# Kernel optimization log

Measured on AMD Instinct MI355X. Metric: run time of the kernel, lower is better.

## Reference

```python
import jax, jax.numpy as jnp
import numpy as np

B, S, D = 2, 2048, 1024
H, L = 16, 64  # num_heads, latent_dim (head dim); head_dim = H*L = 1024
ROPE_BASE = 10000.0


def _rope_tables(seq_len, dim):
    inv_freq = 1.0 / (ROPE_BASE ** (2.0 * jnp.arange(0, dim // 2, dtype=jnp.float32) / dim))
    pos = jnp.arange(seq_len, dtype=jnp.float32)
    ang = pos[:, None] * inv_freq[None, :]           # [S, L/2]
    cos = jnp.cos(ang).reshape(1, seq_len, 1, dim // 2)
    sin = jnp.sin(ang).reshape(1, seq_len, 1, dim // 2)
    return cos, sin


def _apply_rope(t, cos, sin):
    # t: [B, S, H, L]; interleaved-pair rotation then concat halves (as in source)
    tr = t.reshape(*t.shape[:-1], -1, 2)             # [B,S,H,L/2,2]
    x0, x1 = tr[..., 0], tr[..., 1]
    out = jnp.concatenate([x0 * cos - x1 * sin, x0 * sin + x1 * cos], axis=-1)
    return out.reshape(t.shape)


def setup_inputs() -> dict:
    key = jax.random.key(0)
    ks = jax.random.split(key, 5)
    scale = 0.03  # ~xavier for 1024x1024
    return {
        "x": jax.random.normal(ks[0], (B, S, D), dtype=jnp.float32),
        "Wq": jax.random.normal(ks[1], (D, H * L), dtype=jnp.float32) * scale,
        "bq": jnp.zeros((H * L,), dtype=jnp.float32),
        "Wk": jax.random.normal(ks[2], (D, H * L), dtype=jnp.float32) * scale,
        "bk": jnp.zeros((H * L,), dtype=jnp.float32),
        "Wv": jax.random.normal(ks[3], (D, H * L), dtype=jnp.float32) * scale,
        "bv": jnp.zeros((H * L,), dtype=jnp.float32),
        "Wo": jax.random.normal(ks[4], (H * L, D), dtype=jnp.float32) * scale,
        "bo": jnp.zeros((D,), dtype=jnp.float32),
    }


def reference(x, Wq, bq, Wk, bk, Wv, bv, Wo, bo):
    b, s, _ = x.shape
    q = (x @ Wq + bq).reshape(b, s, H, L)
    k = (x @ Wk + bk).reshape(b, s, H, L)
    v = (x @ Wv + bv).reshape(b, s, H, L)
    cos, sin = _rope_tables(s, L)
    q = _apply_rope(q, cos, sin)
    k = _apply_rope(k, cos, sin)
    q = jnp.transpose(q, (0, 2, 1, 3))  # [B,H,S,L]
    k = jnp.transpose(k, (0, 2, 1, 3))
    v = jnp.transpose(v, (0, 2, 1, 3))
    scores = jnp.einsum('bnqd,bnkd->bnqk', q, k) / jnp.sqrt(jnp.float32(L))
    # causal mask: keep positions where key <= query
    causal = jnp.arange(s)[None, :] <= jnp.arange(s)[:, None]  # [S,S]
    scores = jnp.where(causal, scores, -1e9)
    attn = jax.nn.softmax(scores, axis=-1)
    attended = jnp.einsum('bnqk,bnkd->bnqd', attn, v)
    attended = jnp.transpose(attended, (0, 2, 1, 3)).reshape(b, s, H * L)
    return attended @ Wo + bo
```

## Files before the change

### kernel.cpp

```cpp
#include <hip/hip_runtime.h>
#include <hip/hip_bf16.h>

typedef __bf16 bf16_t;
typedef __bf16 bf16x2 __attribute__((ext_vector_type(2)));
typedef __bf16 bf16x4 __attribute__((ext_vector_type(4)));
typedef __bf16 bf16x8 __attribute__((ext_vector_type(8)));
typedef float  f32x4  __attribute__((ext_vector_type(4)));

#define GLDS16(gp, lp) __builtin_amdgcn_global_load_lds( \
    (const __attribute__((address_space(1))) void*)(gp), \
    (__attribute__((address_space(3))) void*)(lp), 16, 0, 0)

#define MFMA16(a, b, c) __builtin_amdgcn_mfma_f32_16x16x32_bf16((a), (b), (c), 0, 0, 0)

static constexpr int kB = 2, kS = 2048, kD = 1024, kH = 16, kL = 64;
static constexpr int kM = kB * kS;
static constexpr int kNqkv = 3 * kD;
static constexpr int kBH = kB * kH;

__global__ __launch_bounds__(256)
void prep_kernel(const float* __restrict__ x, bf16_t* __restrict__ xb,
                 const float* __restrict__ Wq, const float* __restrict__ Wk,
                 const float* __restrict__ Wv, const float* __restrict__ Wo,
                 bf16_t* __restrict__ Wqkv, bf16_t* __restrict__ WoT,
                 float* __restrict__ cosT, float* __restrict__ sinT) {
    const int bid = blockIdx.x;
    const int tid = threadIdx.x;
    if (bid < 4096) {
        int i = bid * 256 + tid;
        float4 v = ((const float4*)x)[i];
        bf16x4 o;
        o[0] = (bf16_t)v.x; o[1] = (bf16_t)v.y; o[2] = (bf16_t)v.z; o[3] = (bf16_t)v.w;
        ((bf16x4*)xb)[i] = o;
    } else if (bid < 8192) {
        __shared__ float t[32 * 33];
        const int wid4 = bid - 4096;
        const int z = wid4 >> 10;
        const int rem = wid4 & 1023;
        const int k0 = (rem & 31) * 32, n0 = (rem >> 5) * 32;
        const float* W = (z == 0) ? Wq : (z == 1) ? Wk : (z == 2) ? Wv : Wo;
        bf16_t* Wt = (z < 3) ? (Wqkv + (size_t)z * 1024 * 1024) : WoT;
#pragma unroll
        for (int i = 0; i < 4; ++i) {
            int idx = i * 256 + tid;
            int r = idx >> 5, c = idx & 31;
            t[r * 33 + c] = W[(size_t)(k0 + r) * 1024 + n0 + c];
        }
        __syncthreads();
#pragma unroll
        for (int i = 0; i < 4; ++i) {
            int idx = i * 256 + tid;
            int r = idx >> 5, c = idx & 31;
            Wt[(size_t)(n0 + r) * 1024 + k0 + c] = (bf16_t)t[c * 33 + r];
        }
    } else {
        int i = (bid - 8192) * 256 + tid;
        int s = i >> 5, j = i & 31;
        double inv = pow(10000.0, -2.0 * (double)j / 64.0);
        double ang = (double)s * inv;
        cosT[i] = (float)cos(ang);
        sinT[i] = (float)sin(ang);
    }
}

template <int MODE>
__global__ __launch_bounds__(256, 2)
void gemm_bf16(const bf16_t* __restrict__ A, const bf16_t* __restrict__ Bt,
               void* __restrict__ Cout,
               const float* __restrict__ b0, const float* __restrict__ b1,
               const float* __restrict__ b2, int Ndim, int Kdim) {
    __shared__ __align__(16) bf16_t Alds[128 * 32];
    __shared__ __align__(16) bf16_t Blds[128 * 32];
    const int tid = threadIdx.x;
    const int lane = tid & 63;
    const int wid = tid >> 6;
    const int lo = lane & 15, hi = lane >> 4;
    const int bm = blockIdx.x, bn = blockIdx.y;
    const int wr = wid >> 1, wc = wid & 1;

    const int rowS = (wid * 2) * 16 + (lane >> 2);
    const int colE = (lane & 3) * 8;
    const bf16_t* gA0 = A + (size_t)(bm * 128 + rowS) * Kdim + colE;
    const bf16_t* gA1 = gA0 + (size_t)16 * Kdim;
    const bf16_t* gB0 = Bt + (size_t)(bn * 128 + rowS) * Kdim + colE;
    const bf16_t* gB1 = gB0 + (size_t)16 * Kdim;
    bf16_t* lA0 = &Alds[(wid * 2) * 512];
    bf16_t* lA1 = &Alds[(wid * 2 + 1) * 512];
    bf16_t* lB0 = &Blds[(wid * 2) * 512];
    bf16_t* lB1 = &Blds[(wid * 2 + 1) * 512];

    f32x4 acc[4][4];
#pragma unroll
    for (int m = 0; m < 4; ++m)
#pragma unroll
        for (int n = 0; n < 4; ++n) acc[m][n] = (f32x4){0.f, 0.f, 0.f, 0.f};

    const int nk = Kdim >> 5;
    for (int kt = 0; kt < nk; ++kt) {
        const int k0 = kt * 32;
        GLDS16(gA0 + k0, lA0);
        GLDS16(gA1 + k0, lA1);
        GLDS16(gB0 + k0, lB0);
        GLDS16(gB1 + k0, lB1);
        __syncthreads();
        bf16x8 aF[4], bF[4];
#pragma unroll
        for (int m = 0; m < 4; ++m)
            aF[m] = *(const bf16x8*)&Alds[(wr * 64 + m * 16 + lo) * 32 + hi * 8];
#pragma unroll
        for (int n = 0; n < 4; ++n)
            bF[n] = *(const bf16x8*)&Blds[(wc * 64 + n * 16 + lo) * 32 + hi * 8];
#pragma unroll
        for (int m = 0; m < 4; ++m)
#pragma unroll
            for (int n = 0; n < 4; ++n)
                acc[m][n] = MFMA16(aF[m], bF[n], acc[m][n]);
        __syncthreads();
    }

    const int rbase = bm * 128 + wr * 64 + hi * 4;
    const int cbase = bn * 128 + wc * 64 + lo;
    if (MODE == 0) {
        bf16_t* C = (bf16_t*)Cout;
#pragma unroll
        for (int m = 0; m < 4; ++m)
#pragma unroll
            for (int n = 0; n < 4; ++n) {
                const int col = cbase + n * 16;
                const float bias = (col < 1024) ? b0[col]
                                 : (col < 2048) ? b1[col - 1024] : b2[col - 2048];
#pragma unroll
                for (int r = 0; r < 4; ++r) {
                    const int row = rbase + m * 16 + r;
                    C[(size_t)row * Ndim + col] = (bf16_t)(acc[m][n][r] + bias);
                }
            }
    } else {
        float* C = (float*)Cout;
#pragma unroll
        for (int m = 0; m < 4; ++m)
#pragma unroll
            for (int n = 0; n < 4; ++n) {
                const int col = cbase + n * 16;
                const float bias = b0[col];
#pragma unroll
                for (int r = 0; r < 4; ++r) {
                    const int row = rbase + m * 16 + r;
                    C[(size_t)row * Ndim + col] = acc[m][n][r] + bias;
                }
            }
    }
}

__global__ __launch_bounds__(256)
void qkvprep_kernel(const bf16_t* __restrict__ qkv,
                    const float* __restrict__ cosT,
                    const float* __restrict__ sinT,
                    bf16_t* __restrict__ Qr, bf16_t* __restrict__ Kr,
                    bf16_t* __restrict__ VT) {
    const int st = blockIdx.x, bh = blockIdx.y;
    const int b = bh >> 4, h = bh & 15;
    const int tid = threadIdx.x;
    {
        const int r = tid >> 2;
        const int part = tid & 3;
        const int s = st * 64 + r;
        const int bs = b * kS + s;
        const bf16_t* qp = qkv + (size_t)bs * kNqkv + h * 64 + part * 16;
        const bf16_t* kp = qp + 1024;
        const size_t outoff = ((size_t)(b * kH + h) * kS + s) * 64;
        bf16_t* qo = Qr + outoff;
        char*   kob = (char*)(Kr + outoff);
        const float* cr = cosT + s * 32 + part * 8;
        const float* sr = sinT + s * 32 + part * 8;
        const float kScale = 0.125f * 1.44269504f;

        bf16x8 q0 = *(const bf16x8*)qp;
        bf16x8 q1 = *(const bf16x8*)(qp + 8);
        bf16x8 k0 = *(const bf16x8*)kp;
        bf16x8 k1 = *(const bf16x8*)(kp + 8);
        bf16x8 qlo, qhi, klo, khi;
#pragma unroll
        for (int j = 0; j < 8; ++j) {
            const float cv = cr[j];
            const float sv = sr[j];
            float qa, qb2, ka, kb2;
            if (j < 4) {
                qa = (float)q0[2 * j];     qb2 = (float)q0[2 * j + 1];
                ka = (float)k0[2 * j];     kb2 = (float)k0[2 * j + 1];
            } else {
                qa = (float)q1[2 * j - 8]; qb2 = (float)q1[2 * j - 7];
                ka = (float)k1[2 * j - 8]; kb2 = (float)k1[2 * j - 7];
            }
            qlo[j] = (bf16_t)((qa * cv - qb2 * sv) * kScale);
            qhi[j] = (bf16_t)((qa * sv + qb2 * cv) * kScale);
            klo[j] = (bf16_t)(ka * cv - kb2 * sv);
            khi[j] = (bf16_t)(ka * sv + kb2 * cv);
        }
        *(bf16x8*)(qo + part * 8)      = qlo;
        *(bf16x8*)(qo + 32 + part * 8) = qhi;
        const int sw = s & 7;
        *(bf16x8*)(kob + (((part)     ^ sw) << 4)) = klo;
        *(bf16x8*)(kob + (((part + 4) ^ sw) << 4)) = khi;
    }
    {
        __shared__ __align__(16) bf16_t t[64 * 72];
        const int r = tid >> 2, g = tid & 3;
        const bf16_t* src = qkv + ((size_t)(b * kS + st * 64 + r)) * kNqkv + 2048 + h * 64 + g * 16;
        bf16x8 v0 = *(const bf16x8*)src;
        bf16x8 v1 = *(const bf16x8*)(src + 8);
        *(bf16x8*)&t[r * 72 + g * 16] = v0;
        *(bf16x8*)&t[r * 72 + g * 16 + 8] = v1;
        __syncthreads();
        bf16x8 o0, o1;
#pragma unroll
        for (int j = 0; j < 8; ++j) {
            o0[j] = t[(g * 16 + j) * 72 + r];
            o1[j] = t[(g * 16 + 8 + j) * 72 + r];
        }
        char* dstb = (char*)(VT + ((size_t)bh * 64 + r) * kS) + st * 128;
        const int sw = r & 7;
        *(bf16x8*)(dstb + (((g * 2)     ^ sw) << 4)) = o0;
        *(bf16x8*)(dstb + (((g * 2 + 1) ^ sw) << 4)) = o1;
    }
}

__global__ __launch_bounds__(256, 4)
void attn_kernel(const bf16_t* __restrict__ Qr, const bf16_t* __restrict__ Kr,
                 const bf16_t* __restrict__ VT, bf16_t* __restrict__ attended) {
    __shared__ __align__(16) bf16_t Klds[2][64 * 64];
    __shared__ __align__(16) bf16_t Vlds[2][64 * 64];
    __shared__ __align__(16) bf16_t Plds[4][16 * 64];
    const int bh = blockIdx.x;
    const int y = blockIdx.y;
    const int qt = (y < 8) ? (31 - y) : (y < 16) ? (y + 8)
                 : (y < 24) ? (31 - y) : (y - 24);
    const int tid = threadIdx.x;
    const int lane = tid & 63, wid = tid >> 6;
    const int lo = lane & 15, hi = lane >> 4;
    const int q0 = qt * 64 + wid * 16;

    const char* Kg = (const char*)(Kr + (size_t)bh * kS * 64);
    const char* Vg = (const char*)(VT + (size_t)bh * 64 * kS);
    const bf16_t* Q = Qr + (size_t)bh * kS * 64;

    const bf16x8 aQ0 = *(const bf16x8*)&Q[(size_t)(q0 + lo) * 64 + hi * 8];
    const bf16x8 aQ1 = *(const bf16x8*)&Q[(size_t)(q0 + lo) * 64 + 32 + hi * 8];

    char* Pb = (char*)&Plds[wid][0];
    const int psw = (lo & 7) << 4;

    f32x4 O[4];
#pragma unroll
    for (int dt = 0; dt < 4; ++dt) O[dt] = (f32x4){0.f, 0.f, 0.f, 0.f};
    float m_run = -1e30f, l_run = 0.f;

    auto stage = [&](int buf, int t) {
        char* Kl = (char*)&Klds[buf][0];
        char* Vl = (char*)&Vlds[buf][0];
        const size_t kb = (size_t)t * 128 * 64;
        const int vcol = t * 128;
#pragma unroll
        for (int j = 0; j < 2; ++j) {
            const int seg = wid * 2 + j;
            GLDS16(Kg + kb + seg * 1024 + lane * 16, Kl + seg * 1024);
            const int row = seg * 8 + (lane >> 3);
            GLDS16(Vg + (size_t)row * (kS * 2) + vcol + (lane & 7) * 16, Vl + seg * 1024);
        }
    };

    stage(0, 0);
    int cur = 0;
    const int ntiles = qt + 1;
    for (int t = 0; t < ntiles; ++t) {
        __syncthreads();
        if (t + 1 < ntiles) stage(cur ^ 1, t + 1);
        const char* Kb = (const char*)&Klds[cur][0];
        const char* Vb = (const char*)&Vlds[cur][0];
        const int kv0 = t * 64;
        const bool edge = (t == qt);

        f32x4 s[4];
#pragma unroll
        for (int ct = 0; ct < 4; ++ct) s[ct] = (f32x4){0.f, 0.f, 0.f, 0.f};
        __builtin_amdgcn_s_setprio(1);
#pragma unroll
        for (int ct = 0; ct < 4; ++ct) {
            const int rr = ct * 16 + lo;
            const bf16x8 bK0 = *(const bf16x8*)(Kb + rr * 128 + (((hi)     ^ (rr & 7)) << 4));
            const bf16x8 bK1 = *(const bf16x8*)(Kb + rr * 128 + (((hi + 4) ^ (rr & 7)) << 4));
            s[ct] = MFMA16(bK0, aQ0, s[ct]);
            s[ct] = MFMA16(bK1, aQ1, s[ct]);
        }
        __builtin_amdgcn_s_setprio(0);

        if (edge) {
            const int qg = q0 + lo;
#pragma unroll
            for (int ct = 0; ct < 4; ++ct)
#pragma unroll
                for (int r = 0; r < 4; ++r)
                    if (kv0 + ct * 16 + hi * 4 + r > qg) s[ct][r] = -1e30f;
        }
        float pmax = -1e30f;
#pragma unroll
        for (int ct = 0; ct < 4; ++ct)
#pragma unroll
            for (int r = 0; r < 4; ++r) pmax = fmaxf(pmax, s[ct][r]);
        pmax = fmaxf(pmax, __shfl_xor(pmax, 16, 64));
        pmax = fmaxf(pmax, __shfl_xor(pmax, 32, 64));
        if (!__all(pmax - m_run <= 8.0f)) {
            const float mn = fmaxf(m_run, pmax);
            const float alpha = exp2f(m_run - mn);
            m_run = mn;
            l_run *= alpha;
            float av[4];
#pragma unroll
            for (int r = 0; r < 4; ++r) av[r] = __shfl(alpha, hi * 4 + r, 64);
#pragma unroll
            for (int dt = 0; dt < 4; ++dt)
#pragma unroll
                for (int r = 0; r < 4; ++r) O[dt][r] *= av[r];
        }
        float psum = 0.f;
#pragma unroll
        for (int ct = 0; ct < 4; ++ct)
#pragma unroll
            for (int r = 0; r < 4; ++r) {
                const float e = exp2f(s[ct][r] - m_run);
                s[ct][r] = e;
                psum += e;
            }
        psum += __shfl_xor(psum, 16, 64);
        psum += __shfl_xor(psum, 32, 64);
        l_run += psum;
#pragma unroll
        for (int ct = 0; ct < 4; ++ct)
#pragma unroll
            for (int rp = 0; rp < 2; ++rp) {
                bf16x2 v;
                v[0] = (bf16_t)s[ct][2 * rp];
                v[1] = (bf16_t)s[ct][2 * rp + 1];
                *(bf16x2*)(Pb + ((lo * 128 + (ct * 16 + hi * 4 + 2 * rp) * 2) ^ psw)) = v;
            }
        const bf16x8 aP0 = *(const bf16x8*)(Pb + ((lo * 128 + hi * 16) ^ psw));
        const bf16x8 aP1 = *(const bf16x8*)(Pb + ((lo * 128 + 64 + hi * 16) ^ psw));

        __builtin_amdgcn_s_setprio(1);
#pragma unroll
        for (int dt = 0; dt < 4; ++dt) {
            const int rr = dt * 16 + lo;
            const bf16x8 bV0 = *(const bf16x8*)(Vb + rr * 128 + (((hi)     ^ (rr & 7)) << 4));
            const bf16x8 bV1 = *(const bf16x8*)(Vb + rr * 128 + (((hi + 4) ^ (rr & 7)) << 4));
            O[dt] = MFMA16(aP0, bV0, O[dt]);
            O[dt] = MFMA16(aP1, bV1, O[dt]);
        }
        __builtin_amdgcn_s_setprio(0);
        cur ^= 1;
    }

    const int b = bh >> 4, h = bh & 15;
    float li[4];
#pragma unroll
    for (int r = 0; r < 4; ++r) li[r] = 1.0f / __shfl(l_run, hi * 4 + r, 64);
#pragma unroll
    for (int dt = 0; dt < 4; ++dt)
#pragma unroll
        for (int r = 0; r < 4; ++r) {
            const int row = q0 + hi * 4 + r;
            attended[((size_t)(b * kS + row)) * kD + h * 64 + dt * 16 + lo] =
                (bf16_t)(O[dt][r] * li[r]);
        }
}

extern "C" void kernel_launch(void* const* d_in, const int* in_sizes, int n_in,
                              void* d_out, int out_size, void* d_ws, size_t ws_size,
                              hipStream_t stream) {
    const float* x  = (const float*)d_in[0];
    const float* Wq = (const float*)d_in[1];
    const float* bq = (const float*)d_in[2];
    const float* Wk = (const float*)d_in[3];
    const float* bk = (const float*)d_in[4];
    const float* Wv = (const float*)d_in[5];
    const float* bv = (const float*)d_in[6];
    const float* Wo = (const float*)d_in[7];
    const float* bo = (const float*)d_in[8];
    float* out = (float*)d_out;

    char* ws = (char*)d_ws;
    size_t off = 0;
    auto carve = [&](size_t bytes) -> char* {
        char* p = ws + off;
        off += (bytes + 255) & ~(size_t)255;
        return p;
    };
    bf16_t* xb    = (bf16_t*)carve((size_t)kM * kD * 2);
    bf16_t* WqkvT = (bf16_t*)carve((size_t)kNqkv * kD * 2);
    bf16_t* WoT   = (bf16_t*)carve((size_t)kD * kD * 2);
    float*  cosT  = (float*)carve((size_t)kS * 32 * 4);
    float*  sinT  = (float*)carve((size_t)kS * 32 * 4);
    bf16_t* qkv   = (bf16_t*)carve((size_t)kM * kNqkv * 2);
    bf16_t* Qr    = (bf16_t*)carve((size_t)kBH * kS * 64 * 2);
    bf16_t* Kr    = (bf16_t*)carve((size_t)kBH * kS * 64 * 2);
    bf16_t* VT    = (bf16_t*)carve((size_t)kBH * kS * 64 * 2);
    bf16_t* att   = (bf16_t*)carve((size_t)kM * kD * 2);

    prep_kernel<<<8448, 256, 0, stream>>>(x, xb, Wq, Wk, Wv, Wo, WqkvT, WoT, cosT, sinT);

    gemm_bf16<0><<<dim3(kM / 128, kNqkv / 128), 256, 0, stream>>>(
        xb, WqkvT, qkv, bq, bk, bv, kNqkv, kD);

    qkvprep_kernel<<<dim3(kS / 64, kBH), 256, 0, stream>>>(qkv, cosT, sinT, Qr, Kr, VT);

    attn_kernel<<<dim3(kBH, 32), 256, 0, stream>>>(Qr, Kr, VT, att);

    gemm_bf16<1><<<dim3(kM / 128, kD / 128), 256, 0, stream>>>(
        att, WoT, out, bo, nullptr, nullptr, kD, kD);
}
```

Measured before the change: 126.0 us.

## Double GEMM K-tile to 64 with XOR-swizzled LDS layout

The bf16 GEMM now stages a 64-wide K slice per iteration instead of 32, which halves the number of loop iterations and barrier pairs. Global-to-LDS loads are rearranged into 8-row segments, with the 16-byte column chunks XOR-swizzled by row so the fragment reads avoid LDS bank conflicts. LDS use per block doubles to 32 KB and more fragment registers are live, which may reduce occupancy. Loads are still not double-buffered.

```diff
diff --git a/kernel.cpp b/kernel.cpp
--- a/kernel.cpp
+++ b/kernel.cpp
@@ -69,8 +69,8 @@
                void* __restrict__ Cout,
                const float* __restrict__ b0, const float* __restrict__ b1,
                const float* __restrict__ b2, int Ndim, int Kdim) {
-    __shared__ __align__(16) bf16_t Alds[128 * 32];
-    __shared__ __align__(16) bf16_t Blds[128 * 32];
+    __shared__ __align__(16) bf16_t Alds[128 * 64];
+    __shared__ __align__(16) bf16_t Blds[128 * 64];
     const int tid = threadIdx.x;
     const int lane = tid & 63;
     const int wid = tid >> 6;
@@ -78,16 +78,9 @@
     const int bm = blockIdx.x, bn = blockIdx.y;
     const int wr = wid >> 1, wc = wid & 1;
 
-    const int rowS = (wid * 2) * 16 + (lane >> 2);
-    const int colE = (lane & 3) * 8;
-    const bf16_t* gA0 = A + (size_t)(bm * 128 + rowS) * Kdim + colE;
-    const bf16_t* gA1 = gA0 + (size_t)16 * Kdim;
-    const bf16_t* gB0 = Bt + (size_t)(bn * 128 + rowS) * Kdim + colE;
-    const bf16_t* gB1 = gB0 + (size_t)16 * Kdim;
-    bf16_t* lA0 = &Alds[(wid * 2) * 512];
-    bf16_t* lA1 = &Alds[(wid * 2 + 1) * 512];
-    bf16_t* lB0 = &Blds[(wid * 2) * 512];
-    bf16_t* lB1 = &Blds[(wid * 2 + 1) * 512];
+    const int rowL = lane >> 3;
+    const int colP = (lane & 7) ^ rowL;
+    const int asw = lo & 7;
 
     f32x4 acc[4][4];
 #pragma unroll
@@ -95,26 +88,43 @@
 #pragma unroll
         for (int n = 0; n < 4; ++n) acc[m][n] = (f32x4){0.f, 0.f, 0.f, 0.f};
 
-    const int nk = Kdim >> 5;
+    auto stage = [&](int kt) {
+        const int k0 = kt * 64;
+#pragma unroll
+        for (int j = 0; j < 4; ++j) {
+            const int seg = wid * 4 + j;
+            const int row = seg * 8 + rowL;
+            GLDS16(A  + (size_t)(bm * 128 + row) * Kdim + k0 + colP * 8,
+                   &Alds[seg * 512 + lane * 8]);
+            GLDS16(Bt + (size_t)(bn * 128 + row) * Kdim + k0 + colP * 8,
+                   &Blds[seg * 512 + lane * 8]);
+        }
+    };
+
+    const int nk = Kdim >> 6;
     for (int kt = 0; kt < nk; ++kt) {
-        const int k0 = kt * 32;
-        GLDS16(gA0 + k0, lA0);
-        GLDS16(gA1 + k0, lA1);
-        GLDS16(gB0 + k0, lB0);
-        GLDS16(gB1 + k0, lB1);
+        stage(kt);
         __syncthreads();
-        bf16x8 aF[4], bF[4];
+        bf16x8 aF0[4], aF1[4], bF0[4], bF1[4];
+#pragma unroll
+        for (int m = 0; m < 4; ++m) {
+            const int R = wr * 64 + m * 16 + lo;
+            aF0[m] = *(const bf16x8*)&Alds[R * 64 + ((hi ^ asw) * 8)];
+            aF1[m] = *(const bf16x8*)&Alds[R * 64 + (((hi + 4) ^ asw) * 8)];
+        }
+#pragma unroll
+        for (int n = 0; n < 4; ++n) {
+            const int R = wc * 64 + n * 16 + lo;
+            bF0[n] = *(const bf16x8*)&Blds[R * 64 + ((hi ^ asw) * 8)];
+            bF1[n] = *(const bf16x8*)&Blds[R * 64 + (((hi + 4) ^ asw) * 8)];
+        }
 #pragma unroll
         for (int m = 0; m < 4; ++m)
-            aF[m] = *(const bf16x8*)&Alds[(wr * 64 + m * 16 + lo) * 32 + hi * 8];
-#pragma unroll
-        for (int n = 0; n < 4; ++n)
-            bF[n] = *(const bf16x8*)&Blds[(wc * 64 + n * 16 + lo) * 32 + hi * 8];
-#pragma unroll
-        for (int m = 0; m < 4; ++m)
-#pragma unroll
-            for (int n = 0; n < 4; ++n)
-                acc[m][n] = MFMA16(aF[m], bF[n], acc[m][n]);
+#pragma unroll
+            for (int n = 0; n < 4; ++n) {
+                acc[m][n] = MFMA16(aF0[m], bF0[n], acc[m][n]);
+                acc[m][n] = MFMA16(aF1[m], bF1[n], acc[m][n]);
+            }
         __syncthreads();
     }
 
```

New measurement: 121.4 us (median of 2 runs). -3.7%, faster.
